# Kernel optimization log

Hardware: AMD Instinct MI355X
Metric: run time of the kernel (lower is better)

Reference implementation:

```python
import jax, jax.numpy as jnp
import numpy as np

NUM_HEADS = 8
HEAD_SIZE = 64


def setup_inputs() -> dict:
    key = jax.random.key(0)
    ks = jax.random.split(key, 7)
    B, P, De, F = 16, 64, 512, 128
    d_model = NUM_HEADS * HEAD_SIZE  # 512
    s = 0.05  # ~ keras RandomNormal default stddev
    return {
        "patch_embeddings": jax.random.normal(ks[0], (B, P, De), jnp.float32),
        "patches_relative_feature": jax.random.normal(ks[1], (B, P, P, F), jnp.float32),
        "patches_relative_mask": jnp.ones((B, P, P), dtype=bool),
        "Wq": jax.random.normal(ks[2], (De, d_model), jnp.float32) * s,
        "Wk": jax.random.normal(ks[3], (De + F, d_model), jnp.float32) * s,
        "Wv": jax.random.normal(ks[4], (De + F, d_model), jnp.float32) * s,
        "Wo": jax.random.normal(ks[5], (d_model, d_model), jnp.float32) * s,
    }


def reference(patch_embeddings, patches_relative_feature, patches_relative_mask, Wq, Wk, Wv, Wo):
    # Vectorized form of the per-patch python loop: for query patch q,
    # keys/values come from concat(patch_embeddings, rel_feature[:, q]).
    B, P, De = patch_embeddings.shape
    H, hs = NUM_HEADS, HEAD_SIZE
    q = (patch_embeddings @ Wq).reshape(B, P, H, hs)  # [B,P,H,hs], seq_len=1 per patch
    # relative key/value inputs: [B, Pq, Pk, De+F]
    rel = jnp.concatenate(
        [jnp.broadcast_to(patch_embeddings[:, None], (B, P, P, De)), patches_relative_feature],
        axis=-1,
    )
    k = (rel @ Wk).reshape(B, P, P, H, hs)
    v = (rel @ Wv).reshape(B, P, P, H, hs)
    scale = 1.0 / jnp.sqrt(jnp.asarray(hs, q.dtype))
    scores = jnp.einsum("bqhd,bqkhd->bqhk", q, k) * scale  # [B,Pq,H,Pk]
    attn = jax.nn.softmax(scores, axis=-1)
    out = jnp.einsum("bqhk,bqkhd->bqhd", attn, v).reshape(B, P, H * hs)
    return out @ Wo  # [B, P, d_model]
```

## Files before the change

kernel.cpp:

```cpp
#include <hip/hip_runtime.h>
#include <hip/hip_bf16.h>


typedef __attribute__((ext_vector_type(8))) short short8;
typedef __attribute__((ext_vector_type(4))) short short4v;
typedef __attribute__((ext_vector_type(4))) float f32x4;

static __device__ __forceinline__ short f2bf(float x) {
  __hip_bfloat16 h = __float2bfloat16(x);
  union { __hip_bfloat16 h; short s; } u;
  u.h = h;
  return u.s;
}
static __device__ __forceinline__ float bf2f(short s) {
  union { unsigned int u; float f; } c;
  c.u = ((unsigned int)(unsigned short)s) << 16;
  return c.f;
}
static __device__ __forceinline__ float bflo(unsigned int u) {
  union { unsigned int u; float f; } c; c.u = u << 16; return c.f;
}
static __device__ __forceinline__ float bfhi(unsigned int u) {
  union { unsigned int u; float f; } c; c.u = u & 0xFFFF0000u; return c.f;
}

__global__ __launch_bounds__(256) void prep(const float* __restrict__ pe,
                                            const float* __restrict__ Wq,
                                            const float* __restrict__ Wk,
                                            const float* __restrict__ Wv,
                                            const float* __restrict__ Wo,
                                            short* __restrict__ pe_bf,
                                            short* __restrict__ Bt,
                                            short* __restrict__ BtO,
                                            short* __restrict__ Wk2t,
                                            short* __restrict__ Wv2bf) {
  __shared__ float t[32][33];
  const int bid = blockIdx.x, tid = threadIdx.x;
  if (bid < 1024) {
    const int np0 = (bid & 63) * 32, k0 = (bid >> 6) * 32;
    const int tx = tid & 31, ty = tid >> 5;
    const int sid = np0 >> 9;
    const float* src = (sid == 0) ? Wq : (sid == 1) ? Wv : (sid == 2) ? Wk : Wo;
    const int nc0 = np0 & 511;
#pragma unroll
    for (int r = 0; r < 4; ++r) {
      int kl = ty + r * 8;
      t[kl][tx] = src[(size_t)(k0 + kl) * 512 + nc0 + tx];
    }
    __syncthreads();
#pragma unroll
    for (int r = 0; r < 4; ++r) {
      int nl = ty + r * 8;
      short bv = f2bf(t[tx][nl]);
      int np = np0 + nl;
      if (np < 1536) Bt[(size_t)np * 512 + k0 + tx] = bv;
      else           BtO[(size_t)(np - 1536) * 512 + k0 + tx] = bv;
    }
  } else if (bid < 1088) {
    const int b2 = bid - 1024;
    const int f0 = (b2 & 3) * 32, e0 = (b2 >> 2) * 32;
    const int tx = tid & 31, ty = tid >> 5;
    const float* Wk2 = Wk + 512 * 512;
#pragma unroll
    for (int r = 0; r < 4; ++r) {
      int fl = ty + r * 8;
      t[fl][tx] = Wk2[(size_t)(f0 + fl) * 512 + e0 + tx];
    }
    __syncthreads();
#pragma unroll
    for (int r = 0; r < 4; ++r) {
      int el = ty + r * 8;
      Wk2t[(size_t)(e0 + el) * 128 + f0 + tx] = f2bf(t[tx][el]);
    }
  } else if (bid < 1152) {
    int i = ((bid - 1088) * 256 + tid) * 4;
    const float* Wv2 = Wv + 512 * 512;
    float4 v = *(const float4*)(Wv2 + i);
    short4v o = {f2bf(v.x), f2bf(v.y), f2bf(v.z), f2bf(v.w)};
    *(short4v*)(Wv2bf + i) = o;
  } else {
    int i = ((bid - 1152) * 256 + tid) * 4;
    float4 v = *(const float4*)(pe + i);
    short4v o = {f2bf(v.x), f2bf(v.y), f2bf(v.z), f2bf(v.w)};
    *(short4v*)(pe_bf + i) = o;
  }
}

__global__ __launch_bounds__(256) void gemm_qkvu(const short* __restrict__ A,
                                                 const short* __restrict__ Bt,
                                                 short* __restrict__ QV,
                                                 short* __restrict__ K0t2) {
  const int wave = threadIdx.x >> 6, lane = threadIdx.x & 63;
  const int wr = wave >> 1, wc = wave & 1;
  const int r = lane & 15, g = lane >> 4;
  const int row0 = blockIdx.x * 64 + wr * 32;
  const int col0 = blockIdx.y * 64 + wc * 32;
  const short8* a0p = (const short8*)(A + (size_t)(row0 + r) * 512 + g * 8);
  const short8* a1p = (const short8*)(A + (size_t)(row0 + 16 + r) * 512 + g * 8);
  const short8* b0p = (const short8*)(Bt + (size_t)(col0 + r) * 512 + g * 8);
  const short8* b1p = (const short8*)(Bt + (size_t)(col0 + 16 + r) * 512 + g * 8);
  f32x4 acc00 = {}, acc01 = {}, acc10 = {}, acc11 = {};
  short8 A0[2][4], A1[2][4], B0[2][4], B1[2][4];
  auto LOAD = [&](int buf, int ss) {
#pragma unroll
    for (int c = 0; c < 4; ++c) {
      A0[buf][c] = a0p[(ss * 4 + c) * 4];
      A1[buf][c] = a1p[(ss * 4 + c) * 4];
      B0[buf][c] = b0p[(ss * 4 + c) * 4];
      B1[buf][c] = b1p[(ss * 4 + c) * 4];
    }
  };
  auto MM = [&](int buf) {
#pragma unroll
    for (int c = 0; c < 4; ++c) {
      acc00 = __builtin_amdgcn_mfma_f32_16x16x32_bf16(A0[buf][c], B0[buf][c], acc00, 0, 0, 0);
      acc01 = __builtin_amdgcn_mfma_f32_16x16x32_bf16(A0[buf][c], B1[buf][c], acc01, 0, 0, 0);
      acc10 = __builtin_amdgcn_mfma_f32_16x16x32_bf16(A1[buf][c], B0[buf][c], acc10, 0, 0, 0);
      acc11 = __builtin_amdgcn_mfma_f32_16x16x32_bf16(A1[buf][c], B1[buf][c], acc11, 0, 0, 0);
    }
  };
  LOAD(0, 0);
  LOAD(1, 1);
  MM(0);
  LOAD(0, 2);
  MM(1);
  LOAD(1, 3);
  MM(0);
  MM(1);
  const int crow = (lane >> 4) * 4, ccol = lane & 15;
  const bool k0sec = (blockIdx.y >= 16);
#pragma unroll
  for (int i = 0; i < 2; ++i)
#pragma unroll
    for (int j = 0; j < 2; ++j) {
      f32x4 a = (i == 0) ? (j == 0 ? acc00 : acc01) : (j == 0 ? acc10 : acc11);
#pragma unroll
      for (int rg = 0; rg < 4; ++rg) {
        size_t row = row0 + i * 16 + crow + rg;
        size_t col = col0 + j * 16 + ccol;
        short v = f2bf(a[rg]);
        if (!k0sec) {
          QV[row * 1024 + col] = v;
        } else {
          size_t c = col - 1024;
          size_t b = row >> 6, kk = row & 63;
          K0t2[((b * 256 + (c >> 1)) * 64 + kk) * 2 + (c & 1)] = v;
        }
      }
    }
}

__global__ __launch_bounds__(256) void gemm_out(const short* __restrict__ A,
                                                const short* __restrict__ Bt,
                                                float* __restrict__ C) {
  const int wave = threadIdx.x >> 6, lane = threadIdx.x & 63;
  const int wr = wave >> 1, wc = wave & 1;
  const int r = lane & 15, g = lane >> 4;
  const int row0 = blockIdx.x * 64 + wr * 32;
  const int col0 = blockIdx.y * 64 + wc * 32;
  const short8* a0p = (const short8*)(A + (size_t)(row0 + r) * 512 + g * 8);
  const short8* a1p = (const short8*)(A + (size_t)(row0 + 16 + r) * 512 + g * 8);
  const short8* b0p = (const short8*)(Bt + (size_t)(col0 + r) * 512 + g * 8);
  const short8* b1p = (const short8*)(Bt + (size_t)(col0 + 16 + r) * 512 + g * 8);
  f32x4 acc00 = {}, acc01 = {}, acc10 = {}, acc11 = {};
  short8 A0[2][4], A1[2][4], B0[2][4], B1[2][4];
  auto LOAD = [&](int buf, int ss) {
#pragma unroll
    for (int c = 0; c < 4; ++c) {
      A0[buf][c] = a0p[(ss * 4 + c) * 4];
      A1[buf][c] = a1p[(ss * 4 + c) * 4];
      B0[buf][c] = b0p[(ss * 4 + c) * 4];
      B1[buf][c] = b1p[(ss * 4 + c) * 4];
    }
  };
  auto MM = [&](int buf) {
#pragma unroll
    for (int c = 0; c < 4; ++c) {
      acc00 = __builtin_amdgcn_mfma_f32_16x16x32_bf16(A0[buf][c], B0[buf][c], acc00, 0, 0, 0);
      acc01 = __builtin_amdgcn_mfma_f32_16x16x32_bf16(A0[buf][c], B1[buf][c], acc01, 0, 0, 0);
      acc10 = __builtin_amdgcn_mfma_f32_16x16x32_bf16(A1[buf][c], B0[buf][c], acc10, 0, 0, 0);
      acc11 = __builtin_amdgcn_mfma_f32_16x16x32_bf16(A1[buf][c], B1[buf][c], acc11, 0, 0, 0);
    }
  };
  LOAD(0, 0);
  LOAD(1, 1);
  MM(0);
  LOAD(0, 2);
  MM(1);
  LOAD(1, 3);
  MM(0);
  MM(1);
  const int crow = (lane >> 4) * 4, ccol = lane & 15;
#pragma unroll
  for (int i = 0; i < 2; ++i)
#pragma unroll
    for (int j = 0; j < 2; ++j) {
      f32x4 a = (i == 0) ? (j == 0 ? acc00 : acc01) : (j == 0 ? acc10 : acc11);
#pragma unroll
      for (int rg = 0; rg < 4; ++rg)
        C[(size_t)(row0 + i * 16 + crow + rg) * 512 + col0 + j * 16 + ccol] = a[rg];
    }
}

__global__ __launch_bounds__(512) void attn_fused(const short* __restrict__ QV,
                                                  const unsigned int* __restrict__ K0t2,
                                                  const float* __restrict__ relf,
                                                  const short* __restrict__ Wk2t,
                                                  const short* __restrict__ Wv2bf,
                                                  short* __restrict__ AO) {
  const int bq = blockIdx.x, b = bq >> 6;
  const int tid = threadIdx.x;
  const int h = tid >> 6, lane = tid & 63;

  __shared__ float relf_s[64][129];
  __shared__ float q_s[512];
  __shared__ float u_s[8][128];
  __shared__ float attn_s[8][64];
  __shared__ float w_s[8][128];

  q_s[tid] = bf2f(QV[(size_t)bq * 1024 + tid]);

  const float* rf = relf + (size_t)bq * 8192;
#pragma unroll
  for (int it = 0; it < 4; ++it) {
    int idx = (it * 512 + tid) * 4;
    float4 gv = *(const float4*)(rf + idx);
    int kk = idx >> 7, f = idx & 127;
    relf_s[kk][f + 0] = gv.x; relf_s[kk][f + 1] = gv.y;
    relf_s[kk][f + 2] = gv.z; relf_s[kk][f + 3] = gv.w;
  }
  __syncthreads();

  {
    const unsigned int* wp = (const unsigned int*)(Wk2t + (size_t)h * 64 * 128) + lane;
    float u0 = 0.f, u1 = 0.f;
#pragma unroll 8
    for (int d = 0; d < 64; ++d) {
      unsigned int uv = wp[d * 64];
      float qd = q_s[h * 64 + d];
      u0 += qd * bflo(uv);
      u1 += qd * bfhi(uv);
    }
    u_s[h][lane * 2] = u0;
    u_s[h][lane * 2 + 1] = u1;
  }

  float s = 0.f;
  {
    const unsigned int* kp = K0t2 + ((size_t)b * 256 + h * 32) * 64 + lane;
#pragma unroll 8
    for (int d2 = 0; d2 < 32; ++d2) {
      unsigned int uv = kp[(size_t)d2 * 64];
      s += q_s[h * 64 + d2 * 2] * bflo(uv) + q_s[h * 64 + d2 * 2 + 1] * bfhi(uv);
    }
#pragma unroll
    for (int f4 = 0; f4 < 32; ++f4) {
      float4 rv = *(const float4*)&relf_s[lane][f4 * 4];
      const float4 uv = *(const float4*)&u_s[h][f4 * 4];
      s += uv.x * rv.x + uv.y * rv.y + uv.z * rv.z + uv.w * rv.w;
    }
    s *= 0.125f;
  }
  float m = s;
#pragma unroll
  for (int off = 32; off; off >>= 1) m = fmaxf(m, __shfl_xor(m, off));
  float p = __expf(s - m);
  float sum = p;
#pragma unroll
  for (int off = 32; off; off >>= 1) sum += __shfl_xor(sum, off);
  attn_s[h][lane] = p / sum;

  {
    float w0 = 0.f, w1 = 0.f;
#pragma unroll 8
    for (int kk = 0; kk < 64; ++kk) {
      float a = attn_s[h][kk];
      w0 += a * relf_s[kk][lane];
      w1 += a * relf_s[kk][lane + 64];
    }
    w_s[h][lane] = w0;
    w_s[h][lane + 64] = w1;
  }

  float o = 0.f;
  {
    const short* v0col = QV + (size_t)(b * 64) * 1024 + 512 + h * 64 + lane;
#pragma unroll 16
    for (int kk = 0; kk < 64; ++kk) o += attn_s[h][kk] * bf2f(v0col[(size_t)kk * 1024]);
    const short* wvcol = Wv2bf + h * 64 + lane;
#pragma unroll 16
    for (int f = 0; f < 128; ++f) o += w_s[h][f] * bf2f(wvcol[(size_t)f * 512]);
  }
  AO[(size_t)bq * 512 + h * 64 + lane] = f2bf(o);
}

extern "C" void kernel_launch(void* const* d_in, const int* in_sizes, int n_in,
                              void* d_out, int out_size, void* d_ws, size_t ws_size,
                              hipStream_t stream) {
  const float* pe   = (const float*)d_in[0];
  const float* relf = (const float*)d_in[1];
  const float* Wq = (const float*)d_in[3];
  const float* Wk = (const float*)d_in[4];
  const float* Wv = (const float*)d_in[5];
  const float* Wo = (const float*)d_in[6];
  float* out = (float*)d_out;

  short* ws = (short*)d_ws;
  short* pe_bf = ws;
  short* Bt    = pe_bf + 524288;
  short* BtO   = Bt + 786432;
  short* Wk2t  = BtO + 262144;
  short* Wv2bf = Wk2t + 65536;
  short* QV    = Wv2bf + 65536;
  short* K0t2  = QV + 1048576;
  short* AObf  = pe_bf;

  prep<<<1664, 256, 0, stream>>>(pe, Wq, Wk, Wv, Wo, pe_bf, Bt, BtO, Wk2t, Wv2bf);
  gemm_qkvu<<<dim3(16, 24), 256, 0, stream>>>(pe_bf, Bt, QV, K0t2);
  attn_fused<<<1024, 512, 0, stream>>>(QV, (const unsigned int*)K0t2, relf, Wk2t, Wv2bf, AObf);
  gemm_out<<<dim3(16, 8), 256, 0, stream>>>(AObf, BtO, out);
}
```

Before: 143.0 us.

## Fuse patch-embedding bf16 conversion into GEMM loads and shrink attention LDS

The separate pe→bf16 conversion pass in prep is removed, and gemm_qkvu now loads fp32 activations directly and converts them in registers. In attn_fused the relative-feature tile is stored in LDS as bf16 instead of fp32, which halves shared memory per block and could allow more resident blocks. Block indices are also remapped to interleave batches across the grid. In exchange the GEMM reads twice the bytes for A, the relf values lose precision, and extra conversion instructions are added.

New measurement: 147.1 us. 2.8% more time.

```diff
diff --git a/kernel.cpp b/kernel.cpp
--- a/kernel.cpp
+++ b/kernel.cpp
@@ -23,13 +23,17 @@
 static __device__ __forceinline__ float bfhi(unsigned int u) {
   union { unsigned int u; float f; } c; c.u = u & 0xFFFF0000u; return c.f;
 }
-
-__global__ __launch_bounds__(256) void prep(const float* __restrict__ pe,
-                                            const float* __restrict__ Wq,
+static __device__ __forceinline__ short8 ldcvt(const float* p) {
+  float4 v0 = *(const float4*)p, v1 = *(const float4*)(p + 4);
+  short8 r = {f2bf(v0.x), f2bf(v0.y), f2bf(v0.z), f2bf(v0.w),
+              f2bf(v1.x), f2bf(v1.y), f2bf(v1.z), f2bf(v1.w)};
+  return r;
+}
+
+__global__ __launch_bounds__(256) void prep(const float* __restrict__ Wq,
                                             const float* __restrict__ Wk,
                                             const float* __restrict__ Wv,
                                             const float* __restrict__ Wo,
-                                            short* __restrict__ pe_bf,
                                             short* __restrict__ Bt,
                                             short* __restrict__ BtO,
                                             short* __restrict__ Wk2t,
@@ -72,21 +76,16 @@
       int el = ty + r * 8;
       Wk2t[(size_t)(e0 + el) * 128 + f0 + tx] = f2bf(t[tx][el]);
     }
-  } else if (bid < 1152) {
+  } else {
     int i = ((bid - 1088) * 256 + tid) * 4;
     const float* Wv2 = Wv + 512 * 512;
     float4 v = *(const float4*)(Wv2 + i);
     short4v o = {f2bf(v.x), f2bf(v.y), f2bf(v.z), f2bf(v.w)};
     *(short4v*)(Wv2bf + i) = o;
-  } else {
-    int i = ((bid - 1152) * 256 + tid) * 4;
-    float4 v = *(const float4*)(pe + i);
-    short4v o = {f2bf(v.x), f2bf(v.y), f2bf(v.z), f2bf(v.w)};
-    *(short4v*)(pe_bf + i) = o;
-  }
-}
-
-__global__ __launch_bounds__(256) void gemm_qkvu(const short* __restrict__ A,
+  }
+}
+
+__global__ __launch_bounds__(256) void gemm_qkvu(const float* __restrict__ A,
                                                  const short* __restrict__ Bt,
                                                  short* __restrict__ QV,
                                                  short* __restrict__ K0t2) {
@@ -95,8 +94,8 @@
   const int r = lane & 15, g = lane >> 4;
   const int row0 = blockIdx.x * 64 + wr * 32;
   const int col0 = blockIdx.y * 64 + wc * 32;
-  const short8* a0p = (const short8*)(A + (size_t)(row0 + r) * 512 + g * 8);
-  const short8* a1p = (const short8*)(A + (size_t)(row0 + 16 + r) * 512 + g * 8);
+  const float* a0f = A + (size_t)(row0 + r) * 512 + g * 8;
+  const float* a1f = A + (size_t)(row0 + 16 + r) * 512 + g * 8;
   const short8* b0p = (const short8*)(Bt + (size_t)(col0 + r) * 512 + g * 8);
   const short8* b1p = (const short8*)(Bt + (size_t)(col0 + 16 + r) * 512 + g * 8);
   f32x4 acc00 = {}, acc01 = {}, acc10 = {}, acc11 = {};
@@ -104,8 +103,8 @@
   auto LOAD = [&](int buf, int ss) {
 #pragma unroll
     for (int c = 0; c < 4; ++c) {
-      A0[buf][c] = a0p[(ss * 4 + c) * 4];
-      A1[buf][c] = a1p[(ss * 4 + c) * 4];
+      A0[buf][c] = ldcvt(a0f + (ss * 4 + c) * 32);
+      A1[buf][c] = ldcvt(a1f + (ss * 4 + c) * 32);
       B0[buf][c] = b0p[(ss * 4 + c) * 4];
       B1[buf][c] = b1p[(ss * 4 + c) * 4];
     }
@@ -208,11 +207,13 @@
                                                   const short* __restrict__ Wk2t,
                                                   const short* __restrict__ Wv2bf,
                                                   short* __restrict__ AO) {
-  const int bq = blockIdx.x, b = bq >> 6;
+  const int orig = blockIdx.x;
+  const int bq = (orig & 7) * 128 + (orig >> 3);
+  const int b = bq >> 6;
   const int tid = threadIdx.x;
   const int h = tid >> 6, lane = tid & 63;
 
-  __shared__ float relf_s[64][129];
+  __shared__ short relf_s[64][136];
   __shared__ float q_s[512];
   __shared__ float u_s[8][128];
   __shared__ float attn_s[8][64];
@@ -226,8 +227,8 @@
     int idx = (it * 512 + tid) * 4;
     float4 gv = *(const float4*)(rf + idx);
     int kk = idx >> 7, f = idx & 127;
-    relf_s[kk][f + 0] = gv.x; relf_s[kk][f + 1] = gv.y;
-    relf_s[kk][f + 2] = gv.z; relf_s[kk][f + 3] = gv.w;
+    short4v o = {f2bf(gv.x), f2bf(gv.y), f2bf(gv.z), f2bf(gv.w)};
+    *(short4v*)&relf_s[kk][f] = o;
   }
   __syncthreads();
 
@@ -254,10 +255,12 @@
       s += q_s[h * 64 + d2 * 2] * bflo(uv) + q_s[h * 64 + d2 * 2 + 1] * bfhi(uv);
     }
 #pragma unroll
-    for (int f4 = 0; f4 < 32; ++f4) {
-      float4 rv = *(const float4*)&relf_s[lane][f4 * 4];
-      const float4 uv = *(const float4*)&u_s[h][f4 * 4];
-      s += uv.x * rv.x + uv.y * rv.y + uv.z * rv.z + uv.w * rv.w;
+    for (int f8 = 0; f8 < 16; ++f8) {
+      short8 rv = *(const short8*)&relf_s[lane][f8 * 8];
+      float4 ua = *(const float4*)&u_s[h][f8 * 8];
+      float4 ub = *(const float4*)&u_s[h][f8 * 8 + 4];
+      s += ua.x * bf2f(rv[0]) + ua.y * bf2f(rv[1]) + ua.z * bf2f(rv[2]) + ua.w * bf2f(rv[3]);
+      s += ub.x * bf2f(rv[4]) + ub.y * bf2f(rv[5]) + ub.z * bf2f(rv[6]) + ub.w * bf2f(rv[7]);
     }
     s *= 0.125f;
   }
@@ -275,8 +278,8 @@
 #pragma unroll 8
     for (int kk = 0; kk < 64; ++kk) {
       float a = attn_s[h][kk];
-      w0 += a * relf_s[kk][lane];
-      w1 += a * relf_s[kk][lane + 64];
+      w0 += a * bf2f(relf_s[kk][lane]);
+      w1 += a * bf2f(relf_s[kk][lane + 64]);
     }
     w_s[h][lane] = w0;
     w_s[h][lane + 64] = w1;
@@ -306,17 +309,16 @@
   float* out = (float*)d_out;
 
   short* ws = (short*)d_ws;
-  short* pe_bf = ws;
-  short* Bt    = pe_bf + 524288;
+  short* Bt    = ws;
   short* BtO   = Bt + 786432;
   short* Wk2t  = BtO + 262144;
   short* Wv2bf = Wk2t + 65536;
   short* QV    = Wv2bf + 65536;
   short* K0t2  = QV + 1048576;
-  short* AObf  = pe_bf;
-
-  prep<<<1664, 256, 0, stream>>>(pe, Wq, Wk, Wv, Wo, pe_bf, Bt, BtO, Wk2t, Wv2bf);
-  gemm_qkvu<<<dim3(16, 24), 256, 0, stream>>>(pe_bf, Bt, QV, K0t2);
+  short* AObf  = K0t2 + 524288;
+
+  prep<<<1152, 256, 0, stream>>>(Wq, Wk, Wv, Wo, Bt, BtO, Wk2t, Wv2bf);
+  gemm_qkvu<<<dim3(16, 24), 256, 0, stream>>>(pe, Bt, QV, K0t2);
   attn_fused<<<1024, 512, 0, stream>>>(QV, (const unsigned int*)K0t2, relf, Wk2t, Wv2bf, AObf);
   gemm_out<<<dim3(16, 8), 256, 0, stream>>>(AObf, BtO, out);
 }
```
